# Optimization experiments

Measured on AMD Instinct MI355X. Metric: run time of the kernel, lower is better.

Reference implementation:

```python
import jax, jax.numpy as jnp
import numpy as np

B, S, D = 8, 1024, 1024
H, DK, DV = 16, 64, 64
EPS = 1e-5


def gaussian_prior(n_heads, len_q, len_k):
    # per-head causal Gaussian bias: exp(-(i-j)^2 / (2*sigma_h^2)) for i>=j else 0
    i = jnp.arange(len_q)[:, None]
    j = jnp.arange(len_k)[None, :]
    dist2 = (i - j).astype(jnp.float32) ** 2              # [S, S]
    sigma = jnp.arange(1, n_heads + 1, dtype=jnp.float32) # sigma_h = h+1
    bias = jnp.exp(-dist2[None] / (2.0 * sigma[:, None, None] ** 2))  # [H, S, S]
    return jnp.where(i >= j, bias, 0.0)


def setup_inputs() -> dict:
    key = jax.random.key(0)
    ks = jax.random.split(key, 7)
    input_Q = jax.random.normal(ks[0], (B, S, D), dtype=jnp.float32)
    input_K = jax.random.normal(ks[1], (B, S, D), dtype=jnp.float32)
    input_V = jax.random.normal(ks[2], (B, S, D), dtype=jnp.float32)
    # causal mask: True where attention is disallowed (j > i)
    causal = jnp.triu(jnp.ones((S, S), dtype=bool), k=1)
    attn_mask = jnp.broadcast_to(causal, (B, S, S))
    scale = 0.02
    Wq = jax.random.normal(ks[3], (H * DK, D), dtype=jnp.float32) * scale  # torch Linear weight [out,in]
    Wk = jax.random.normal(ks[4], (H * DK, D), dtype=jnp.float32) * scale
    Wv = jax.random.normal(ks[5], (H * DV, D), dtype=jnp.float32) * scale
    Wfc = jax.random.normal(ks[6], (D, H * DV), dtype=jnp.float32) * scale
    return {"input_Q": input_Q, "input_K": input_K, "input_V": input_V,
            "attn_mask": attn_mask, "Wq": Wq, "Wk": Wk, "Wv": Wv, "Wfc": Wfc}


def reference(input_Q, input_K, input_V, attn_mask, Wq, Wk, Wv, Wfc):
    b, s, d = input_Q.shape
    residual = input_Q
    # projections -> [B, H, S, dk]
    Q = (input_Q @ Wq.T).reshape(b, s, H, DK).transpose(0, 2, 1, 3)
    K = (input_K @ Wk.T).reshape(b, s, H, DK).transpose(0, 2, 1, 3)
    V = (input_V @ Wv.T).reshape(b, s, H, DV).transpose(0, 2, 1, 3)
    scores = jnp.einsum("bhqd,bhkd->bhqk", Q, K) / jnp.sqrt(jnp.float32(DK))
    scores = scores + gaussian_prior(H, s, s)[None]        # add Gaussian positional bias
    scores = jnp.where(attn_mask[:, None], -1e9, scores)   # masked_fill_
    attn = jax.nn.softmax(scores, axis=-1)
    context = jnp.einsum("bhqk,bhkd->bhqd", attn, V)
    context = context.transpose(0, 2, 1, 3).reshape(b, s, H * DV)
    output = context @ Wfc.T
    x = output + residual
    # LayerNorm (fresh module each call in source -> weight=1, bias=0)
    mu = jnp.mean(x, axis=-1, keepdims=True)
    var = jnp.var(x, axis=-1, keepdims=True)
    out = (x - mu) * jax.lax.rsqrt(var + EPS)
    return out, attn
```

## Files before the change

kernel.cpp:

```cpp
#include <hip/hip_runtime.h>
#include <hip/hip_bf16.h>

#define NP 8388608

typedef __attribute__((ext_vector_type(8))) short short8;
typedef __attribute__((ext_vector_type(4))) float f32x4;

__device__ __forceinline__ ushort f2bf(float f) {
  union { float f; unsigned u; } v; v.f = f;
  unsigned r = v.u + 0x7fffu + ((v.u >> 16) & 1u);
  return (ushort)(r >> 16);
}

__device__ __forceinline__ void gload16(const void* g, void* l) {
  __builtin_amdgcn_global_load_lds((const __attribute__((address_space(1))) void*)g,
                                   (__attribute__((address_space(3))) void*)l, 16, 0, 0);
}

__global__ void cast_inputs(const float* __restrict__ a, const float* __restrict__ b,
                            const float* __restrict__ c, ushort* __restrict__ dst) {
  const float* src = (blockIdx.y == 0) ? a : (blockIdx.y == 1) ? b : c;
  ushort* d = dst + (size_t)blockIdx.y * NP;
  size_t i = ((size_t)blockIdx.x * 256 + threadIdx.x) * 4;
  f32x4 v = *(const f32x4*)(src + i);
  ushort4 o; o.x = f2bf(v[0]); o.y = f2bf(v[1]); o.z = f2bf(v[2]); o.w = f2bf(v[3]);
  *(ushort4*)(d + i) = o;
}

__global__ void cast_weights(const float* __restrict__ w0, const float* __restrict__ w1,
                             const float* __restrict__ w2, const float* __restrict__ w3,
                             ushort* __restrict__ dst) {
  const float* src = (blockIdx.y == 0) ? w0 : (blockIdx.y == 1) ? w1
                    : (blockIdx.y == 2) ? w2 : w3;
  ushort* d = dst + (size_t)blockIdx.y * 1048576;
  size_t i = ((size_t)blockIdx.x * 256 + threadIdx.x) * 4;
  f32x4 v = *(const f32x4*)(src + i);
  ushort4 o; o.x = f2bf(v[0]); o.y = f2bf(v[1]); o.z = f2bf(v[2]); o.w = f2bf(v[3]);
  *(ushort4*)(d + i) = o;
}

template<int EPI>
__global__ __launch_bounds__(256) void gemm_bt(const ushort* __restrict__ Abase,
                                               const ushort* __restrict__ Bbase,
                                               float* __restrict__ Cf32,
                                               ushort* __restrict__ Qh,
                                               ushort* __restrict__ Kh,
                                               ushort* __restrict__ VhT) {
  constexpr int K = 1024;
  __shared__ ushort As[4096];
  __shared__ ushort Bs[4096];
  const int t = threadIdx.x, w = t >> 6, l = t & 63;
  const int o  = blockIdx.y * 8 + blockIdx.x;
  const int o2 = (o & 7) * 64 + (o >> 3);
  const int n0 = (o2 & 7) * 128, m0 = (o2 >> 3) * 128;
  const int z = blockIdx.z;
  const ushort* A  = Abase + (EPI == 0 ? (size_t)z * NP : 0);
  const ushort* Bm = Bbase + (EPI == 0 ? (size_t)z * 1048576 : 0);

  f32x4 acc[4][4];
#pragma unroll
  for (int i = 0; i < 4; i++)
#pragma unroll
    for (int j = 0; j < 4; j++) acc[i][j] = f32x4{0.f, 0.f, 0.f, 0.f};

  const int wm = w >> 1, wn = w & 1;
  const int arow = w * 16 + (l >> 2);
  const int acol = (l & 3) * 8;
  const int fr = l & 15, fq = l >> 4, fk = fq * 8;

  for (int k0 = 0; k0 < K; k0 += 32) {
    __syncthreads();
#pragma unroll
    for (int r = 0; r < 2; r++) {
      gload16(A  + (size_t)(m0 + r * 64 + arow) * K + k0 + acol, &As[r * 2048 + w * 512]);
      gload16(Bm + (size_t)(n0 + r * 64 + arow) * K + k0 + acol, &Bs[r * 2048 + w * 512]);
    }
    __syncthreads();
    short8 av[4], bv[4];
#pragma unroll
    for (int i = 0; i < 4; i++) {
      av[i] = *(const short8*)&As[(wm * 64 + i * 16 + fr) * 32 + fk];
      bv[i] = *(const short8*)&Bs[(wn * 64 + i * 16 + fr) * 32 + fk];
    }
#pragma unroll
    for (int i = 0; i < 4; i++)
#pragma unroll
      for (int j = 0; j < 4; j++)
        acc[i][j] = __builtin_amdgcn_mfma_f32_16x16x32_bf16(av[i], bv[j], acc[i][j], 0, 0, 0);
  }

#pragma unroll
  for (int i = 0; i < 4; i++)
#pragma unroll
    for (int j = 0; j < 4; j++)
#pragma unroll
      for (int reg = 0; reg < 4; reg++) {
        int m = m0 + wm * 64 + i * 16 + fq * 4 + reg;
        int n = n0 + wn * 64 + j * 16 + fr;
        float v = acc[i][j][reg];
        if (EPI == 1) {
          Cf32[(size_t)m * 1024 + n] = v;
        } else {
          int b = m >> 10, s = m & 1023, h = n >> 6, d = n & 63;
          if (z == 0)
            Qh[((size_t)(b * 16 + h) * 1024 + s) * 64 + d] = f2bf(v * 0.125f);
          else if (z == 1)
            Kh[((size_t)(b * 16 + h) * 1024 + s) * 64 + d] = f2bf(v);
          else
            VhT[((size_t)(b * 16 + h) * 64 + d) * 1024 + s] = f2bf(v);
        }
      }
}

__global__ __launch_bounds__(256) void attn_fused(const ushort* __restrict__ Qh,
                                                  const ushort* __restrict__ Kh,
                                                  const ushort* __restrict__ VhT,
                                                  float* __restrict__ attnO,
                                                  ushort* __restrict__ ctx) {
  __shared__ ushort Kt[2][4096];
  __shared__ ushort Vt[4096];
  __shared__ ushort Pl[4096];
  __shared__ float  biasl[1024];

  const int t = threadIdx.x, w = t >> 6, l = t & 63;
  const int o = blockIdx.x + 8 * blockIdx.y + 128 * blockIdx.z;
  const int gx = (o >> 3) & 7;
  const int bhid = (o & 7) + 8 * (o >> 6);
  const int h = bhid & 15, b = bhid >> 4;
  const size_t bh = (size_t)b * 16 + h;
  const int fr = l & 15, fq = l >> 4, fk = fq * 8;

  const float sig = (float)(h + 1);
  const float minv = -1.0f / (2.0f * sig * sig);
  for (int d = t; d < 1024; d += 256) {
    float fd = (float)d;
    biasl[d] = __expf(fd * fd * minv);
  }

  const int srow = w * 8 + (l >> 3);
  const int sc = l & 7;
  char* Prow = (char*)(Pl + w * 1024 + fr * 64);
  const int pswz = (fr & 7) << 4;

  auto stageK = [&](int kt, int bsel) {
#pragma unroll
    for (int r = 0; r < 2; r++) {
      int row = r * 32 + srow;
      int col = (sc ^ (row & 7)) * 8;
      gload16(Kh + (bh * 1024 + kt * 64 + row) * 64 + col, &Kt[bsel][r * 2048 + w * 512]);
    }
  };
  auto stageV = [&](int kt) {
#pragma unroll
    for (int r = 0; r < 2; r++) {
      int row = r * 32 + srow;
      int col = (sc ^ (row & 7)) * 8;
      gload16(VhT + (bh * 64 + row) * 1024 + kt * 64 + col, &Vt[r * 2048 + w * 512]);
    }
  };

  for (int half = 0; half < 2; half++) {
    const int qt = half ? 15 - gx : gx;
    const int q0 = qt * 64;
    const int qrow_g = q0 + w * 16 + fr;

    const ushort* qrow = Qh + (bh * 1024 + qrow_g) * 64;
    short8 qa0 = *(const short8*)(qrow + fk);
    short8 qa1 = *(const short8*)(qrow + 32 + fk);

    float psum = 0.f;
    stageK(0, 0);
    asm volatile("s_waitcnt vmcnt(0) lgkmcnt(0)" ::: "memory");
    __builtin_amdgcn_s_barrier();
    for (int kt = 0; kt <= qt; kt++) {
      const int cur = kt & 1;
      if (kt < qt) stageK(kt + 1, cur ^ 1);
      __builtin_amdgcn_sched_barrier(0);
#pragma unroll
      for (int cb = 0; cb < 4; cb++) {
        int krow = cb * 16 + fr;
        short8 kb0 = *(const short8*)&Kt[cur][krow * 64 + ((fq ^ (krow & 7)) * 8)];
        short8 kb1 = *(const short8*)&Kt[cur][krow * 64 + (((fq + 4) ^ (krow & 7)) * 8)];
        f32x4 s = f32x4{0.f, 0.f, 0.f, 0.f};
        s = __builtin_amdgcn_mfma_f32_16x16x32_bf16(kb0, qa0, s, 0, 0, 0);
        s = __builtin_amdgcn_mfma_f32_16x16x32_bf16(kb1, qa1, s, 0, 0, 0);
        int kbase = kt * 64 + cb * 16 + fq * 4;
#pragma unroll
        for (int reg = 0; reg < 4; reg++) {
          int dd = qrow_g - (kbase + reg);
          float bb = biasl[max(dd, 0)];
          float p = __expf(s[reg] + bb);
          if (dd >= 0) psum += p;
        }
      }
      asm volatile("s_waitcnt vmcnt(0)" ::: "memory");
      __builtin_amdgcn_s_barrier();
    }
    psum += __shfl_xor(psum, 16, 64);
    psum += __shfl_xor(psum, 32, 64);
    const float linv = 1.0f / psum;

    f32x4 cacc[4];
#pragma unroll
    for (int nb = 0; nb < 4; nb++) cacc[nb] = f32x4{0.f, 0.f, 0.f, 0.f};

    float* arow_p = attnO + (bh * 1024 + qrow_g) * 1024;

    stageK(0, 0);
    asm volatile("s_waitcnt vmcnt(0)" ::: "memory");
    __builtin_amdgcn_s_barrier();
    for (int kt = 0; kt <= qt; kt++) {
      const int cur = kt & 1;
      stageV(kt);
      if (kt < qt) stageK(kt + 1, cur ^ 1);
      __builtin_amdgcn_sched_barrier(0);

#pragma unroll
      for (int cb = 0; cb < 4; cb++) {
        int krow = cb * 16 + fr;
        short8 kb0 = *(const short8*)&Kt[cur][krow * 64 + ((fq ^ (krow & 7)) * 8)];
        short8 kb1 = *(const short8*)&Kt[cur][krow * 64 + (((fq + 4) ^ (krow & 7)) * 8)];
        f32x4 s = f32x4{0.f, 0.f, 0.f, 0.f};
        s = __builtin_amdgcn_mfma_f32_16x16x32_bf16(kb0, qa0, s, 0, 0, 0);
        s = __builtin_amdgcn_mfma_f32_16x16x32_bf16(kb1, qa1, s, 0, 0, 0);
        int kbase = kt * 64 + cb * 16 + fq * 4;
        f32x4 o;
#pragma unroll
        for (int reg = 0; reg < 4; reg++) {
          int dd = qrow_g - (kbase + reg);
          float bb = biasl[max(dd, 0)];
          float p = __expf(s[reg] + bb) * linv;
          o[reg] = (dd >= 0) ? p : 0.0f;
        }
        *(f32x4*)(arow_p + kbase) = o;
        uint2 pk;
        asm("v_cvt_pk_bf16_f32 %0, %1, %2" : "=v"(pk.x) : "v"(o[0]), "v"(o[1]));
        asm("v_cvt_pk_bf16_f32 %0, %1, %2" : "=v"(pk.y) : "v"(o[2]), "v"(o[3]));
        *(uint2*)(Prow + (((cb * 32 + fq * 8) ^ pswz))) = pk;
      }

      if (kt < qt) { asm volatile("s_waitcnt vmcnt(6) lgkmcnt(0)" ::: "memory"); }
      else         { asm volatile("s_waitcnt vmcnt(4) lgkmcnt(0)" ::: "memory"); }
      __builtin_amdgcn_s_barrier();
      __builtin_amdgcn_sched_barrier(0);

      short8 pa0 = *(const short8*)(Prow + ((fq * 16) ^ pswz));
      short8 pa1 = *(const short8*)(Prow + ((64 + fq * 16) ^ pswz));
#pragma unroll
      for (int nb = 0; nb < 4; nb++) {
        int vrow = nb * 16 + fr;
        short8 vb0 = *(const short8*)&Vt[vrow * 64 + ((fq ^ (vrow & 7)) * 8)];
        short8 vb1 = *(const short8*)&Vt[vrow * 64 + (((fq + 4) ^ (vrow & 7)) * 8)];
        cacc[nb] = __builtin_amdgcn_mfma_f32_16x16x32_bf16(pa0, vb0, cacc[nb], 0, 0, 0);
        cacc[nb] = __builtin_amdgcn_mfma_f32_16x16x32_bf16(pa1, vb1, cacc[nb], 0, 0, 0);
      }

      asm volatile("s_waitcnt vmcnt(4)" ::: "memory");
      __builtin_amdgcn_s_barrier();
    }

    int cstart = (qt + 1) * 64;
    if (cstart < 1024) {
      int W4 = (1024 - cstart) >> 2;
      for (int r = w; r < 64; r += 4) {
        float* dst = attnO + (bh * 1024 + q0 + r) * 1024 + cstart;
        for (int c = l; c < W4; c += 64)
          __builtin_nontemporal_store(f32x4{0.f, 0.f, 0.f, 0.f}, (f32x4*)dst + c);
      }
    }

#pragma unroll
    for (int nb = 0; nb < 4; nb++)
#pragma unroll
      for (int reg = 0; reg < 4; reg++) {
        int s = q0 + w * 16 + fq * 4 + reg;
        int col = h * 64 + nb * 16 + fr;
        ctx[((size_t)b * 1024 + s) * 1024 + col] = f2bf(cacc[nb][reg]);
      }
  }
}

__global__ __launch_bounds__(256) void ln_kernel(const float* __restrict__ fc,
                                                 const float* __restrict__ resid,
                                                 float* __restrict__ out) {
  const int row = blockIdx.x, t = threadIdx.x, w = t >> 6, l = t & 63;
  f32x4 xf = *(const f32x4*)(fc    + (size_t)row * 1024 + t * 4);
  f32x4 xr = *(const f32x4*)(resid + (size_t)row * 1024 + t * 4);
  f32x4 x;
#pragma unroll
  for (int i = 0; i < 4; i++) x[i] = xf[i] + xr[i];
  float s1 = x[0] + x[1] + x[2] + x[3];
  float s2 = x[0]*x[0] + x[1]*x[1] + x[2]*x[2] + x[3]*x[3];
#pragma unroll
  for (int off = 1; off < 64; off <<= 1) {
    s1 += __shfl_xor(s1, off, 64);
    s2 += __shfl_xor(s2, off, 64);
  }
  __shared__ float red[8];
  if (l == 0) { red[w] = s1; red[4 + w] = s2; }
  __syncthreads();
  float S1 = red[0] + red[1] + red[2] + red[3];
  float S2 = red[4] + red[5] + red[6] + red[7];
  float mu = S1 * (1.0f / 1024.0f);
  float var = S2 * (1.0f / 1024.0f) - mu * mu;
  float rs = rsqrtf(var + 1e-5f);
  f32x4 o;
#pragma unroll
  for (int i = 0; i < 4; i++) o[i] = (x[i] - mu) * rs;
  *(f32x4*)(out + (size_t)row * 1024 + t * 4) = o;
}

extern "C" void kernel_launch(void* const* d_in, const int* in_sizes, int n_in,
                              void* d_out, int out_size, void* d_ws, size_t ws_size,
                              hipStream_t stream) {
  const float* inQ = (const float*)d_in[0];
  const float* inK = (const float*)d_in[1];
  const float* inV = (const float*)d_in[2];
  const float* Wq  = (const float*)d_in[4];
  const float* Wk  = (const float*)d_in[5];
  const float* Wv  = (const float*)d_in[6];
  const float* Wfc = (const float*)d_in[7];
  float* out   = (float*)d_out;
  float* attnO = out + (size_t)NP;

  char* wsb = (char*)d_ws;
  ushort* Wb   = (ushort*)wsb;
  ushort* inXb = (ushort*)(wsb + 8388608ull);
  ushort* Qh   = (ushort*)(wsb + 58720256ull);
  ushort* Kh   = (ushort*)(wsb + 75497472ull);
  ushort* VhT  = (ushort*)(wsb + 92274688ull);
  ushort* ctx  = (ushort*)(wsb + 8388608ull);
  float*  fcO  = (float*)(wsb + 25165824ull);

  cast_inputs <<<dim3(8192, 3), 256, 0, stream>>>(inQ, inK, inV, inXb);
  cast_weights<<<dim3(1024, 4), 256, 0, stream>>>(Wq, Wk, Wv, Wfc, Wb);
  gemm_bt<0>  <<<dim3(8, 64, 3), 256, 0, stream>>>(inXb, Wb, nullptr, Qh, Kh, VhT);
  attn_fused  <<<dim3(8, 16, 8), 256, 0, stream>>>(Qh, Kh, VhT, attnO, ctx);
  gemm_bt<1>  <<<dim3(8, 64, 1), 256, 0, stream>>>(ctx, Wb + 3145728, fcO,
                                                   nullptr, nullptr, nullptr);
  ln_kernel   <<<8192, 256, 0, stream>>>(fcO, inQ, out);
}
```

Before: 299.8 us.

## Deepen GEMM K-tile to 64 with swizzled LDS, vectorize epilogue, add MFMA priority hints

The projection GEMM now stages a 64-wide K slice per iteration into doubled LDS buffers. An XOR swizzle on the column chunk is meant to avoid bank conflicts, and the change halves the number of barrier pairs per K loop. MFMA operands are swapped so each lane holds four consecutive N outputs, which lets the epilogue write f32x4 and ushort4 vectors instead of scalar stores. The attention kernel also wraps its MFMA blocks in s_setprio to favour matrix issue. Costs are larger LDS usage per block, which may lower occupancy, and VhT stores that stay strided.

```diff
diff --git a/kernel.cpp b/kernel.cpp
--- a/kernel.cpp
+++ b/kernel.cpp
@@ -47,8 +47,8 @@
                                                ushort* __restrict__ Kh,
                                                ushort* __restrict__ VhT) {
   constexpr int K = 1024;
-  __shared__ ushort As[4096];
-  __shared__ ushort Bs[4096];
+  __shared__ ushort As[8192];
+  __shared__ ushort Bs[8192];
   const int t = threadIdx.x, w = t >> 6, l = t & 63;
   const int o  = blockIdx.y * 8 + blockIdx.x;
   const int o2 = (o & 7) * 64 + (o >> 3);
@@ -64,52 +64,65 @@
     for (int j = 0; j < 4; j++) acc[i][j] = f32x4{0.f, 0.f, 0.f, 0.f};
 
   const int wm = w >> 1, wn = w & 1;
-  const int arow = w * 16 + (l >> 2);
-  const int acol = (l & 3) * 8;
-  const int fr = l & 15, fq = l >> 4, fk = fq * 8;
-
-  for (int k0 = 0; k0 < K; k0 += 32) {
+  const int srow = w * 8 + (l >> 3);
+  const int sc = l & 7;
+  const int fr = l & 15, fq = l >> 4;
+  const int fswz = fr & 7;
+
+  for (int k0 = 0; k0 < K; k0 += 64) {
     __syncthreads();
 #pragma unroll
-    for (int r = 0; r < 2; r++) {
-      gload16(A  + (size_t)(m0 + r * 64 + arow) * K + k0 + acol, &As[r * 2048 + w * 512]);
-      gload16(Bm + (size_t)(n0 + r * 64 + arow) * K + k0 + acol, &Bs[r * 2048 + w * 512]);
+    for (int r = 0; r < 4; r++) {
+      int row = r * 32 + srow;
+      int col = (sc ^ (row & 7)) * 8;
+      gload16(A  + (size_t)(m0 + row) * K + k0 + col, &As[r * 2048 + w * 512]);
+      gload16(Bm + (size_t)(n0 + row) * K + k0 + col, &Bs[r * 2048 + w * 512]);
     }
     __syncthreads();
-    short8 av[4], bv[4];
-#pragma unroll
-    for (int i = 0; i < 4; i++) {
-      av[i] = *(const short8*)&As[(wm * 64 + i * 16 + fr) * 32 + fk];
-      bv[i] = *(const short8*)&Bs[(wn * 64 + i * 16 + fr) * 32 + fk];
-    }
-#pragma unroll
-    for (int i = 0; i < 4; i++)
-#pragma unroll
-      for (int j = 0; j < 4; j++)
-        acc[i][j] = __builtin_amdgcn_mfma_f32_16x16x32_bf16(av[i], bv[j], acc[i][j], 0, 0, 0);
-  }
-
-#pragma unroll
-  for (int i = 0; i < 4; i++)
-#pragma unroll
-    for (int j = 0; j < 4; j++)
-#pragma unroll
-      for (int reg = 0; reg < 4; reg++) {
-        int m = m0 + wm * 64 + i * 16 + fq * 4 + reg;
-        int n = n0 + wn * 64 + j * 16 + fr;
-        float v = acc[i][j][reg];
-        if (EPI == 1) {
-          Cf32[(size_t)m * 1024 + n] = v;
+#pragma unroll
+    for (int s2 = 0; s2 < 2; s2++) {
+      short8 av[4], bv[4];
+      const int ck = ((s2 * 4 + fq) ^ fswz) * 8;
+#pragma unroll
+      for (int i = 0; i < 4; i++) {
+        av[i] = *(const short8*)&As[(wm * 64 + i * 16 + fr) * 64 + ck];
+        bv[i] = *(const short8*)&Bs[(wn * 64 + i * 16 + fr) * 64 + ck];
+      }
+#pragma unroll
+      for (int i = 0; i < 4; i++)
+#pragma unroll
+        for (int j = 0; j < 4; j++)
+          acc[i][j] = __builtin_amdgcn_mfma_f32_16x16x32_bf16(bv[j], av[i], acc[i][j], 0, 0, 0);
+    }
+  }
+
+#pragma unroll
+  for (int i = 0; i < 4; i++) {
+    int m = m0 + wm * 64 + i * 16 + fr;
+#pragma unroll
+    for (int j = 0; j < 4; j++) {
+      int n = n0 + wn * 64 + j * 16 + fq * 4;
+      f32x4 v = acc[i][j];
+      if (EPI == 1) {
+        *(f32x4*)(Cf32 + (size_t)m * 1024 + n) = v;
+      } else {
+        int b = m >> 10, s = m & 1023, h = n >> 6, d = n & 63;
+        if (z == 0) {
+          ushort4 q; q.x = f2bf(v[0] * 0.125f); q.y = f2bf(v[1] * 0.125f);
+          q.z = f2bf(v[2] * 0.125f); q.w = f2bf(v[3] * 0.125f);
+          *(ushort4*)(Qh + ((size_t)(b * 16 + h) * 1024 + s) * 64 + d) = q;
+        } else if (z == 1) {
+          ushort4 q; q.x = f2bf(v[0]); q.y = f2bf(v[1]);
+          q.z = f2bf(v[2]); q.w = f2bf(v[3]);
+          *(ushort4*)(Kh + ((size_t)(b * 16 + h) * 1024 + s) * 64 + d) = q;
         } else {
-          int b = m >> 10, s = m & 1023, h = n >> 6, d = n & 63;
-          if (z == 0)
-            Qh[((size_t)(b * 16 + h) * 1024 + s) * 64 + d] = f2bf(v * 0.125f);
-          else if (z == 1)
-            Kh[((size_t)(b * 16 + h) * 1024 + s) * 64 + d] = f2bf(v);
-          else
-            VhT[((size_t)(b * 16 + h) * 64 + d) * 1024 + s] = f2bf(v);
+#pragma unroll
+          for (int reg = 0; reg < 4; reg++)
+            VhT[((size_t)(b * 16 + h) * 64 + d + reg) * 1024 + s] = f2bf(v[reg]);
         }
       }
+    }
+  }
 }
 
 __global__ __launch_bounds__(256) void attn_fused(const ushort* __restrict__ Qh,
@@ -182,8 +195,10 @@
         short8 kb0 = *(const short8*)&Kt[cur][krow * 64 + ((fq ^ (krow & 7)) * 8)];
         short8 kb1 = *(const short8*)&Kt[cur][krow * 64 + (((fq + 4) ^ (krow & 7)) * 8)];
         f32x4 s = f32x4{0.f, 0.f, 0.f, 0.f};
+        __builtin_amdgcn_s_setprio(1);
         s = __builtin_amdgcn_mfma_f32_16x16x32_bf16(kb0, qa0, s, 0, 0, 0);
         s = __builtin_amdgcn_mfma_f32_16x16x32_bf16(kb1, qa1, s, 0, 0, 0);
+        __builtin_amdgcn_s_setprio(0);
         int kbase = kt * 64 + cb * 16 + fq * 4;
 #pragma unroll
         for (int reg = 0; reg < 4; reg++) {
@@ -221,8 +236,10 @@
         short8 kb0 = *(const short8*)&Kt[cur][krow * 64 + ((fq ^ (krow & 7)) * 8)];
         short8 kb1 = *(const short8*)&Kt[cur][krow * 64 + (((fq + 4) ^ (krow & 7)) * 8)];
         f32x4 s = f32x4{0.f, 0.f, 0.f, 0.f};
+        __builtin_amdgcn_s_setprio(1);
         s = __builtin_amdgcn_mfma_f32_16x16x32_bf16(kb0, qa0, s, 0, 0, 0);
         s = __builtin_amdgcn_mfma_f32_16x16x32_bf16(kb1, qa1, s, 0, 0, 0);
+        __builtin_amdgcn_s_setprio(0);
         int kbase = kt * 64 + cb * 16 + fq * 4;
         f32x4 o;
 #pragma unroll
@@ -246,6 +263,7 @@
 
       short8 pa0 = *(const short8*)(Prow + ((fq * 16) ^ pswz));
       short8 pa1 = *(const short8*)(Prow + ((64 + fq * 16) ^ pswz));
+      __builtin_amdgcn_s_setprio(1);
 #pragma unroll
       for (int nb = 0; nb < 4; nb++) {
         int vrow = nb * 16 + fr;
@@ -254,6 +272,7 @@
         cacc[nb] = __builtin_amdgcn_mfma_f32_16x16x32_bf16(pa0, vb0, cacc[nb], 0, 0, 0);
         cacc[nb] = __builtin_amdgcn_mfma_f32_16x16x32_bf16(pa1, vb1, cacc[nb], 0, 0, 0);
       }
+      __builtin_amdgcn_s_setprio(0);
 
       asm volatile("s_waitcnt vmcnt(4)" ::: "memory");
       __builtin_amdgcn_s_barrier();
```

Measured after the change: 276.2 us. 1.09x faster.
